# Optimization experiments

Measured on AMD Instinct MI355X. Metric: run time of the kernel, lower is better.

The kernel has to match this reference:

```python
import jax, jax.numpy as jnp
import numpy as np

K = 7            # neighborhood kernel size
HEADS = 4
DIMS = [64, 64, 64, 64]
POOL = 2
MLP_NAT = 4      # mlp_ratio for NAT layers
MLP_GA = 3       # mlp_ratio for GlobalAttention


def _ln(x, g, b, eps=1e-5):
    m = x.mean(-1, keepdims=True)
    v = ((x - m) ** 2).mean(-1, keepdims=True)
    return (x - m) * jax.lax.rsqrt(v + eps) * g + b


def _nbr(L, k):
    # NATTEN-style clamped window: start in [0, L-k]
    i = jnp.arange(L)
    start = jnp.clip(i - k // 2, 0, L - k)
    idx = start[:, None] + jnp.arange(k)          # [L,k] neighbor coords
    rel = idx - i[:, None] + (k - 1)              # [L,k] rpb index in [0,2k-2]
    return idx, rel


def _nat_attn(x, qkv_w, qkv_b, rpb, proj_w, proj_b):
    B, H, W, C = x.shape
    d = C // HEADS
    qkv = (x @ qkv_w + qkv_b).reshape(B, H, W, 3, HEADS, d)
    q = qkv[..., 0, :, :].transpose(0, 3, 1, 2, 4) * (d ** -0.5)  # [B,h,H,W,d]
    kk = qkv[..., 1, :, :].transpose(0, 3, 1, 2, 4)
    vv = qkv[..., 2, :, :].transpose(0, 3, 1, 2, 4)
    iy, ry = _nbr(H, K)
    ix, rx = _nbr(W, K)
    k_nb = kk[:, :, iy][:, :, :, :, ix]   # [B,h,H,K,W,K,d]
    v_nb = vv[:, :, iy][:, :, :, :, ix]
    attn = jnp.einsum('bhijd,bhiajcd->bhijac', q, k_nb)  # [B,h,H,W,K,K]
    bias = rpb[:, ry][:, :, :, rx]                        # [h,H,K,W,K]
    attn = attn + bias.transpose(0, 1, 3, 2, 4)[None]
    B_, h_, H_, W_ = attn.shape[:4]
    attn = jax.nn.softmax(attn.reshape(B_, h_, H_, W_, K * K), axis=-1)
    attn = attn.reshape(B_, h_, H_, W_, K, K)
    out = jnp.einsum('bhijac,bhiajcd->bhijd', attn, v_nb)
    out = out.transpose(0, 2, 3, 1, 4).reshape(B, H, W, C)
    return out @ proj_w + proj_b


def _nat_block(x, ln1g, ln1b, qw, qb, rpb, pw, pb, ln2g, ln2b, f1w, f1b, f2w, f2b):
    x = x + _nat_attn(_ln(x, ln1g, ln1b), qw, qb, rpb, pw, pb)
    h = _ln(x, ln2g, ln2b)
    h = jax.nn.gelu(h @ f1w + f1b, approximate=False) @ f2w + f2b
    return x + h


def _global_block(x, ln1g, ln1b, qw, qb, ln2g, ln2b, f1w, f1b, f2w, f2b):
    B, H, W, C = x.shape
    d = C // HEADS
    xn = _ln(x, ln1g, ln1b)
    Hp, Wp = H // POOL, W // POOL
    xa = xn.reshape(B, Hp, POOL, Wp, POOL, C).mean((2, 4)).reshape(B, Hp * Wp, C)
    N = Hp * Wp
    qkv = (xa @ qw + qb).reshape(B, N, 3, HEADS, d).transpose(2, 0, 3, 1, 4)
    q, k, v = qkv[0] * (d ** -0.5), qkv[1], qkv[2]
    attn = jax.nn.softmax(jnp.einsum('bhnd,bhmd->bhnm', q, k), axis=-1)
    o = jnp.einsum('bhnm,bhmd->bhnd', attn, v)            # [B,h,N,d]
    o = o.transpose(0, 1, 3, 2).reshape(B, C, Hp, Wp)      # (attn@v).transpose(2,3).reshape(B,C,N)
    o = jnp.repeat(jnp.repeat(o, POOL, axis=2), POOL, axis=3)  # nearest upsample
    x = x + o.transpose(0, 2, 3, 1)
    h = _ln(x, ln2g, ln2b)
    h = jax.nn.gelu(h @ f1w + f1b, approximate=False) @ f2w + f2b
    return x + h


def setup_inputs() -> dict:
    key = jax.random.key(0)
    ks = iter(jax.random.split(key, 32))
    B, H, W = 4, 56, 56
    C = DIMS[0]
    n = len(DIMS) - 1  # 3 NAT branches
    s = 0.02
    inp = {
        'x': jax.random.normal(next(ks), (B, H, W, sum(DIMS)), jnp.float32),
        'nat_ln1_g': jnp.ones((n, C)), 'nat_ln1_b': jnp.zeros((n, C)),
        'nat_qkv_w': jax.random.normal(next(ks), (n, C, 3 * C)) * s,
        'nat_qkv_b': jnp.zeros((n, 3 * C)),
        'nat_rpb': jax.random.normal(next(ks), (n, HEADS, 2 * K - 1, 2 * K - 1)) * s,
        'nat_proj_w': jax.random.normal(next(ks), (n, C, C)) * s,
        'nat_proj_b': jnp.zeros((n, C)),
        'nat_ln2_g': jnp.ones((n, C)), 'nat_ln2_b': jnp.zeros((n, C)),
        'nat_fc1_w': jax.random.normal(next(ks), (n, C, MLP_NAT * C)) * s,
        'nat_fc1_b': jnp.zeros((n, MLP_NAT * C)),
        'nat_fc2_w': jax.random.normal(next(ks), (n, MLP_NAT * C, C)) * s,
        'nat_fc2_b': jnp.zeros((n, C)),
        'ga_ln1_g': jnp.ones((C,)), 'ga_ln1_b': jnp.zeros((C,)),
        'ga_qkv_w': jax.random.normal(next(ks), (C, 3 * C)) * s,
        'ga_qkv_b': jnp.zeros((3 * C,)),
        'ga_ln2_g': jnp.ones((C,)), 'ga_ln2_b': jnp.zeros((C,)),
        'ga_fc1_w': jax.random.normal(next(ks), (C, MLP_GA * C)) * s,
        'ga_fc1_b': jnp.zeros((MLP_GA * C,)),
        'ga_fc2_w': jax.random.normal(next(ks), (MLP_GA * C, C)) * s,
        'ga_fc2_b': jnp.zeros((C,)),
    }
    return inp


def reference(x, nat_ln1_g, nat_ln1_b, nat_qkv_w, nat_qkv_b, nat_rpb, nat_proj_w,
              nat_proj_b, nat_ln2_g, nat_ln2_b, nat_fc1_w, nat_fc1_b, nat_fc2_w,
              nat_fc2_b, ga_ln1_g, ga_ln1_b, ga_qkv_w, ga_qkv_b, ga_ln2_g,
              ga_ln2_b, ga_fc1_w, ga_fc1_b, ga_fc2_w, ga_fc2_b):
    parts = jnp.split(x, np.cumsum(DIMS)[:-1].tolist(), axis=-1)
    outs = []
    for i in range(len(DIMS) - 1):
        outs.append(_nat_block(parts[i], nat_ln1_g[i], nat_ln1_b[i], nat_qkv_w[i],
                               nat_qkv_b[i], nat_rpb[i], nat_proj_w[i], nat_proj_b[i],
                               nat_ln2_g[i], nat_ln2_b[i], nat_fc1_w[i], nat_fc1_b[i],
                               nat_fc2_w[i], nat_fc2_b[i]))
    outs.append(_global_block(parts[-1], ga_ln1_g, ga_ln1_b, ga_qkv_w, ga_qkv_b,
                              ga_ln2_g, ga_ln2_b, ga_fc1_w, ga_fc1_b, ga_fc2_w, ga_fc2_b))
    return jnp.concatenate(outs, axis=-1)
```

## Files before the change

kernel.cpp:

```cpp
#include <hip/hip_runtime.h>
#include <hip/hip_bf16.h>
#include <cstdint>

namespace {

constexpr int NPIX = 12544;

typedef __attribute__((ext_vector_type(8))) short bf16x8;
typedef __attribute__((ext_vector_type(4))) float f32x4;
typedef __attribute__((ext_vector_type(16))) float f32x16;
typedef _Float16 h2 __attribute__((ext_vector_type(2)));

__device__ __forceinline__ float wsum(float v) {
#pragma unroll
  for (int m = 32; m; m >>= 1) v += __shfl_xor(v, m, 64);
  return v;
}

__device__ __forceinline__ uint16_t f2bf(float f) {
  uint32_t u = __builtin_bit_cast(uint32_t, f);
  u += 0x7fffu + ((u >> 16) & 1u);
  return (uint16_t)(u >> 16);
}
__device__ __forceinline__ uint32_t packbf(float a, float b) {
  return (uint32_t)f2bf(a) | ((uint32_t)f2bf(b) << 16);
}
__device__ __forceinline__ ushort f2h(float f) {
  _Float16 h = (_Float16)f;
  return __builtin_bit_cast(ushort, h);
}
__device__ __forceinline__ h2 bch2(uint32_t u) { return __builtin_bit_cast(h2, u); }

__device__ __forceinline__ float gelu_fast(float v) {
  float u = 0.7978845608028654f * (v + 0.044715f * v * v * v);
  float e = __expf(2.f * u);
  float th = 1.f - 2.f * __builtin_amdgcn_rcpf(e + 1.f);
  return 0.5f * v * (1.f + th);
}

__global__ __launch_bounds__(256) void k_prep(
    const float* __restrict__ nqkv, const float* __restrict__ nproj,
    const float* __restrict__ nf1, const float* __restrict__ nf2,
    const float* __restrict__ gqkv, const float* __restrict__ gf1,
    const float* __restrict__ gf2, ushort* __restrict__ wT) {
  int t = blockIdx.x * 256 + threadIdx.x;
  if (t >= 201728) return;
  int i = t;
  if (i < 41472) {
    int br = i / 13824, r = i % 13824, n = r / 72, k = r % 72;
    wT[t] = k < 64 ? f2bf(nqkv[(br * 64 + k) * 192 + n]) : (ushort)0;
    return;
  }
  i -= 41472;
  if (i < 13824) {
    int br = i / 4608, r = i % 4608, n = r / 72, k = r % 72;
    wT[t] = k < 64 ? f2bf(nproj[(br * 64 + k) * 64 + n]) : (ushort)0;
    return;
  }
  i -= 13824;
  if (i < 55296) {
    int br = i / 18432, r = i % 18432, n = r / 72, k = r % 72;
    wT[t] = k < 64 ? f2bf(nf1[(br * 64 + k) * 256 + n]) : (ushort)0;
    return;
  }
  i -= 55296;
  if (i < 50688) {
    int br = i / 16896, r = i % 16896, n = r / 264, k = r % 264;
    wT[t] = k < 256 ? f2bf(nf2[(br * 256 + k) * 64 + n]) : (ushort)0;
    return;
  }
  i -= 50688;
  if (i < 13824) {
    int n = i / 72, k = i % 72;
    wT[t] = k < 64 ? f2bf(gqkv[k * 192 + n]) : (ushort)0;
    return;
  }
  i -= 13824;
  if (i < 13824) {
    int n = i / 72, k = i % 72;
    wT[t] = k < 64 ? f2bf(gf1[k * 192 + n]) : (ushort)0;
    return;
  }
  i -= 13824;
  {
    int n = i / 200, k = i % 200;
    wT[t] = k < 192 ? f2bf(gf2[k * 64 + n]) : (ushort)0;
  }
}

__global__ __launch_bounds__(256) void k_qkv(
    const float* __restrict__ x, const float* __restrict__ nat_ln1_g,
    const float* __restrict__ nat_ln1_b, const ushort* __restrict__ wT,
    const float* __restrict__ nat_qkv_b, ushort* __restrict__ qn,
    ushort* __restrict__ kvn, const float* __restrict__ ga_ln1_g,
    const float* __restrict__ ga_ln1_b, const float* __restrict__ ga_qkv_b,
    ushort* __restrict__ qb, ushort* __restrict__ kb, ushort* __restrict__ vT) {
  __shared__ __align__(16) ushort sA[64 * 72];
  int bid = blockIdx.x;
  int tid = threadIdx.x, lane = tid & 63, wid = tid >> 6;
  if (bid == 637) {
    for (int i = tid; i < 4096; i += 256) {
      int bh = i >> 8, rem = i & 255;
      int n = 784 + (rem >> 4), d = rem & 15;
      qb[((size_t)bh * 800 + n) * 16 + d] = 0;
      kb[((size_t)bh * 800 + n) * 16 + d] = 0;
      vT[((size_t)bh * 16 + d) * 800 + n] = 0;
    }
    return;
  }
  int lr = lane & 15, lk = (lane >> 4) * 8;
  if (bid < 588) {
    int br = bid / 196, grp = bid % 196;
    const ushort* Wg = wT + br * 13824;
    float g = nat_ln1_g[br * 64 + lane], bb = nat_ln1_b[br * 64 + lane];
#pragma unroll
    for (int i = 0; i < 16; ++i) {
      int pl = wid * 16 + i;
      float v = x[(size_t)(grp * 64 + pl) * 256 + br * 64 + lane];
      float s1 = wsum(v), s2 = wsum(v * v);
      float m = s1 * (1.f / 64.f);
      float var = s2 * (1.f / 64.f) - m * m;
      sA[pl * 72 + lane] = f2bf((v - m) * rsqrtf(var + 1e-5f) * g + bb);
    }
    __syncthreads();
    int m0 = wid * 16;
    bf16x8 a0 = *(const bf16x8*)&sA[(m0 + lr) * 72 + lk];
    bf16x8 a1 = *(const bf16x8*)&sA[(m0 + lr) * 72 + 32 + lk];
    int r0 = m0 + (lane >> 4) * 4;
#pragma unroll
    for (int nt = 0; nt < 12; ++nt) {
      int n0 = nt * 16;
      bf16x8 b0 = *(const bf16x8*)&Wg[(n0 + lr) * 72 + lk];
      bf16x8 b1 = *(const bf16x8*)&Wg[(n0 + lr) * 72 + 32 + lk];
      f32x4 acc = {0.f, 0.f, 0.f, 0.f};
      acc = __builtin_amdgcn_mfma_f32_16x16x32_bf16(a0, b0, acc, 0, 0, 0);
      acc = __builtin_amdgcn_mfma_f32_16x16x32_bf16(a1, b1, acc, 0, 0, 0);
      int col = n0 + lr;
      float bias = nat_qkv_b[br * 192 + col];
      if (nt < 4) {
        ushort* op = qn + ((size_t)br * NPIX + grp * 64 + r0) * 64 + col;
#pragma unroll
        for (int r = 0; r < 4; ++r) op[r * 64] = f2h((acc[r] + bias) * 0.25f);
      } else {
        ushort* op = kvn + ((size_t)br * NPIX + grp * 64 + r0) * 128 + (col - 64);
#pragma unroll
        for (int r = 0; r < 4; ++r) op[r * 128] = f2h(acc[r] + bias);
      }
    }
  } else {
    int g64 = bid - 588;
    const ushort* Wg = wT + 161280;
    float gg = ga_ln1_g[lane], bb = ga_ln1_b[lane];
#pragma unroll
    for (int i = 0; i < 16; ++i) {
      int tl = wid * 16 + i;
      int token = g64 * 64 + tl;
      int b = token / 784, rem2 = token % 784, hp = rem2 / 28, wp = rem2 % 28;
      float s = 0.f;
#pragma unroll
      for (int dy = 0; dy < 2; ++dy)
#pragma unroll
        for (int dxx = 0; dxx < 2; ++dxx) {
          int pix = b * 3136 + (hp * 2 + dy) * 56 + (wp * 2 + dxx);
          float v = x[(size_t)pix * 256 + 192 + lane];
          float s1 = wsum(v), s2 = wsum(v * v);
          float m = s1 * (1.f / 64.f);
          float var = s2 * (1.f / 64.f) - m * m;
          s += (v - m) * rsqrtf(var + 1e-5f) * gg + bb;
        }
      sA[tl * 72 + lane] = f2bf(0.25f * s);
    }
    __syncthreads();
    int m0 = wid * 16;
    bf16x8 a0 = *(const bf16x8*)&sA[(m0 + lr) * 72 + lk];
    bf16x8 a1 = *(const bf16x8*)&sA[(m0 + lr) * 72 + 32 + lk];
    int r0 = m0 + (lane >> 4) * 4;
#pragma unroll
    for (int nt = 0; nt < 12; ++nt) {
      int n0 = nt * 16;
      bf16x8 b0 = *(const bf16x8*)&Wg[(n0 + lr) * 72 + lk];
      bf16x8 b1 = *(const bf16x8*)&Wg[(n0 + lr) * 72 + 32 + lk];
      f32x4 acc = {0.f, 0.f, 0.f, 0.f};
      acc = __builtin_amdgcn_mfma_f32_16x16x32_bf16(a0, b0, acc, 0, 0, 0);
      acc = __builtin_amdgcn_mfma_f32_16x16x32_bf16(a1, b1, acc, 0, 0, 0);
      int col = n0 + lr;
      float bias = ga_qkv_b[col];
      int hh = (col & 63) >> 4, d = col & 15;
#pragma unroll
      for (int r = 0; r < 4; ++r) {
        int token = g64 * 64 + r0 + r;
        int b = token / 784, nn = token % 784;
        float v = acc[r] + bias;
        if (col < 64)
          qb[((size_t)(b * 4 + hh) * 800 + nn) * 16 + d] = f2bf(v * 0.25f);
        else if (col < 128)
          kb[((size_t)(b * 4 + hh) * 800 + nn) * 16 + d] = f2bf(v);
        else
          vT[((size_t)(b * 4 + hh) * 16 + d) * 800 + nn] = f2bf(v);
      }
    }
  }
}

__global__ __launch_bounds__(256) void k_attn(
    const ushort* __restrict__ qn, const ushort* __restrict__ kvn,
    const float* __restrict__ rpb, const ushort* __restrict__ wT,
    const float* __restrict__ pb, const float* __restrict__ x,
    float* __restrict__ x1, const ushort* __restrict__ qb,
    const ushort* __restrict__ kb, const ushort* __restrict__ vT,
    float* __restrict__ x1g) {
  __shared__ __align__(16) ushort sBuf[196 * 136];
  int bid = blockIdx.x;
  int tid = threadIdx.x, lane = tid & 63, wid = tid >> 6;
  if (bid < 588) {
    ushort* sKV = sBuf;
    int br = bid / 196, rem = bid % 196;
    int b = rem / 49, t = rem % 49;
    int y0 = (t / 7) * 8, x0 = (t % 7) * 8;
    int hy = min(max(y0 - 3, 0), 42), hx = min(max(x0 - 3, 0), 42);
    const ushort* kvbase = kvn + ((size_t)br * NPIX + b * 3136) * 128;
    for (int i = tid; i < 3136; i += 256) {
      int p = i >> 4, c = i & 15;
      int py = p / 14, px = p % 14;
      int gp = (hy + py) * 56 + (hx + px);
      uint4 v = *(const uint4*)&kvbase[(size_t)gp * 128 + c * 8];
      *(uint4*)&sKV[p * 136 + c * 8] = v;
    }
    __syncthreads();
    int pl = tid & 63, h = tid >> 6;
    int ly = pl >> 3, lx = pl & 7;
    int y = y0 + ly, xg = x0 + lx;
    int sy = min(max(y - 3, 0), 49), sx = min(max(xg - 3, 0), 49);
    int by = sy - hy, bx = sx - hx;
    int gpix = b * 3136 + y * 56 + xg;
    const ushort* qp = qn + ((size_t)br * NPIX + gpix) * 64 + h * 16;
    uint4 qv0 = *(const uint4*)&qp[0];
    uint4 qv1 = *(const uint4*)&qp[8];
    h2 q[8] = {bch2(qv0.x), bch2(qv0.y), bch2(qv0.z), bch2(qv0.w),
               bch2(qv1.x), bch2(qv1.y), bch2(qv1.z), bch2(qv1.w)};
    const float* rp = rpb + (br * 4 + h) * 169 + (sy - y + 6) * 13 + (sx - xg + 6);
    float m = -1e30f, l = 0.f;
    h2 acc[8];
    h2 z = {(_Float16)0.f, (_Float16)0.f};
#pragma unroll
    for (int i = 0; i < 8; ++i) acc[i] = z;
    for (int a = 0; a < 7; ++a) {
      const ushort* krow = &sKV[((by + a) * 14 + bx) * 136 + h * 16];
      for (int c = 0; c < 7; ++c) {
        const ushort* kp = krow + c * 136;
        uint4 k0 = *(const uint4*)&kp[0];
        uint4 k1 = *(const uint4*)&kp[8];
        h2 d = z;
        d = bch2(k0.x) * q[0] + d;
        d = bch2(k0.y) * q[1] + d;
        d = bch2(k0.z) * q[2] + d;
        d = bch2(k0.w) * q[3] + d;
        d = bch2(k1.x) * q[4] + d;
        d = bch2(k1.y) * q[5] + d;
        d = bch2(k1.z) * q[6] + d;
        d = bch2(k1.w) * q[7] + d;
        float sd = (float)d[0] + (float)d[1] + rp[a * 13 + c];
        if (sd > m) {
          float sc = __expf(m - sd);
          m = sd; l *= sc;
          h2 sc2 = {(_Float16)sc, (_Float16)sc};
#pragma unroll
          for (int i = 0; i < 8; ++i) acc[i] = acc[i] * sc2;
        }
        float p = __expf(sd - m);
        l += p;
        h2 p2 = {(_Float16)p, (_Float16)p};
        uint4 v0 = *(const uint4*)&kp[64];
        uint4 v1 = *(const uint4*)&kp[72];
        acc[0] = bch2(v0.x) * p2 + acc[0];
        acc[1] = bch2(v0.y) * p2 + acc[1];
        acc[2] = bch2(v0.z) * p2 + acc[2];
        acc[3] = bch2(v0.w) * p2 + acc[3];
        acc[4] = bch2(v1.x) * p2 + acc[4];
        acc[5] = bch2(v1.y) * p2 + acc[5];
        acc[6] = bch2(v1.z) * p2 + acc[6];
        acc[7] = bch2(v1.w) * p2 + acc[7];
      }
    }
    float inv = 1.f / l;
    __syncthreads();
    ushort* sAp = sBuf;
    uint32_t* ao = (uint32_t*)&sAp[pl * 72 + h * 16];
#pragma unroll
    for (int i = 0; i < 8; ++i)
      ao[i] = packbf((float)acc[i][0] * inv, (float)acc[i][1] * inv);
    __syncthreads();
    const ushort* Wp = wT + 41472 + br * 4608;
    int lr = lane & 15, lk = (lane >> 4) * 8;
    int m0 = wid * 16;
    bf16x8 a0 = *(const bf16x8*)&sAp[(m0 + lr) * 72 + lk];
    bf16x8 a1 = *(const bf16x8*)&sAp[(m0 + lr) * 72 + 32 + lk];
    int r0 = m0 + (lane >> 4) * 4;
#pragma unroll
    for (int nt = 0; nt < 4; ++nt) {
      int n0 = nt * 16;
      bf16x8 b0 = *(const bf16x8*)&Wp[(n0 + lr) * 72 + lk];
      bf16x8 b1 = *(const bf16x8*)&Wp[(n0 + lr) * 72 + 32 + lk];
      f32x4 oacc = {0.f, 0.f, 0.f, 0.f};
      oacc = __builtin_amdgcn_mfma_f32_16x16x32_bf16(a0, b0, oacc, 0, 0, 0);
      oacc = __builtin_amdgcn_mfma_f32_16x16x32_bf16(a1, b1, oacc, 0, 0, 0);
      int col = n0 + lr;
      float bias = pb[br * 64 + col];
#pragma unroll
      for (int r = 0; r < 4; ++r) {
        int rr = r0 + r;
        int gp2 = b * 3136 + (y0 + (rr >> 3)) * 56 + (x0 + (rr & 7));
        x1[((size_t)br * NPIX + gp2) * 64 + col] =
            oacc[r] + bias + x[(size_t)gp2 * 256 + br * 64 + col];
      }
    }
  } else {
    int wt = (bid - 588) * 4 + wid;
    int bh = wt / 25, qt = wt % 25;
    int h = bh & 3, b = bh >> 2;
    int qrow = lane & 31, hi = lane >> 5;
    int dmod = lane & 15;
    const ushort* qbase = qb + (size_t)bh * 800 * 16;
    const ushort* kbase = kb + (size_t)bh * 800 * 16;
    const ushort* vbase = vT + (size_t)bh * 16 * 800 + (size_t)dmod * 800;
    bf16x8 qf = *(const bf16x8*)&qbase[(qt * 32 + qrow) * 16 + hi * 8];
    float m = -1e30f, l = 0.f;
    f32x16 acc_o;
#pragma unroll
    for (int r = 0; r < 16; ++r) acc_o[r] = 0.f;
    bf16x8 kf = *(const bf16x8*)&kbase[(0 + qrow) * 16 + hi * 8];
    bf16x8 vf0 = *(const bf16x8*)&vbase[0 + hi * 8];
    bf16x8 vf1 = *(const bf16x8*)&vbase[16 + hi * 8];
    for (int kt = 0; kt < 25; ++kt) {
      int nb = (kt < 24 ? kt + 1 : 24) * 32;
      bf16x8 nkf = *(const bf16x8*)&kbase[(nb + qrow) * 16 + hi * 8];
      bf16x8 nvf0 = *(const bf16x8*)&vbase[nb + hi * 8];
      bf16x8 nvf1 = *(const bf16x8*)&vbase[nb + 16 + hi * 8];
      f32x16 zero;
#pragma unroll
      for (int r = 0; r < 16; ++r) zero[r] = 0.f;
      f32x16 st = __builtin_amdgcn_mfma_f32_32x32x16_bf16(kf, qf, zero, 0, 0, 0);
      float s[16];
#pragma unroll
      for (int r = 0; r < 16; ++r) s[r] = st[r];
      if (kt == 24) {
#pragma unroll
        for (int r = 8; r < 16; ++r) s[r] = -1e30f;
      }
      float tm = s[0];
#pragma unroll
      for (int r = 1; r < 16; ++r) tm = fmaxf(tm, s[r]);
      tm = fmaxf(tm, __shfl_xor(tm, 32, 64));
      if (__any(tm > m + 8.f)) {
        float mn = fmaxf(m, tm);
        float sc = __expf(m - mn);
        l *= sc;
        m = mn;
#pragma unroll
        for (int r = 0; r < 16; ++r) {
          int row = (r & 3) + 4 * hi + 8 * (r >> 2);
          float scr = __shfl(sc, row, 64);
          acc_o[r] *= scr;
        }
      }
      uint32_t pk[8];
      float ps = 0.f;
#pragma unroll
      for (int i = 0; i < 8; ++i) {
        float p0 = __expf(s[2 * i] - m), p1 = __expf(s[2 * i + 1] - m);
        ps += p0 + p1;
        pk[i] = packbf(p0, p1);
      }
      l += ps;
#pragma unroll
      for (int t = 0; t < 2; ++t) {
        uint32_t c0 = pk[4 * t + 0], c1 = pk[4 * t + 1];
        uint32_t c2 = pk[4 * t + 2], c3 = pk[4 * t + 3];
        uint32_t b00 = __shfl((int)c0, qrow, 64), b02 = __shfl((int)c2, qrow, 64);
        uint32_t b10 = __shfl((int)c1, qrow, 64), b12 = __shfl((int)c3, qrow, 64);
        uint32_t b20 = __shfl((int)c0, qrow + 32, 64), b22 = __shfl((int)c2, qrow + 32, 64);
        uint32_t b30 = __shfl((int)c1, qrow + 32, 64), b32 = __shfl((int)c3, qrow + 32, 64);
        union { uint32_t u[4]; bf16x8 v; } pa;
        pa.u[0] = hi ? b02 : b00;
        pa.u[1] = hi ? b12 : b10;
        pa.u[2] = hi ? b22 : b20;
        pa.u[3] = hi ? b32 : b30;
        acc_o = __builtin_amdgcn_mfma_f32_32x32x16_bf16(pa.v, (t ? vf1 : vf0),
                                                        acc_o, 0, 0, 0);
      }
      kf = nkf; vf0 = nvf0; vf1 = nvf1;
    }
    l += __shfl_xor(l, 32, 64);
    float inv = 1.f / l;
#pragma unroll
    for (int r = 0; r < 16; ++r) {
      int row = (r & 3) + 4 * hi + 8 * (r >> 2);
      float invr = __shfl(inv, row, 64);
      int n = qt * 32 + row;
      if (n < 784 && qrow < 16) {
        float o = acc_o[r] * invr;
        int hp = n / 28, wp = n % 28;
        int ch = h * 16 + dmod;
#pragma unroll
        for (int dy = 0; dy < 2; ++dy)
#pragma unroll
          for (int dxx = 0; dxx < 2; ++dxx) {
            int pix = b * 3136 + (hp * 2 + dy) * 56 + (wp * 2 + dxx);
            x1g[(size_t)pix * 64 + ch] = x[(size_t)pix * 256 + 192 + ch] + o;
          }
      }
    }
  }
}

template <bool NAT>
__device__ __forceinline__ void mlp_body(
    int br, int grp, ushort* sX, ushort* sH,
    const float* __restrict__ x1, const ushort* __restrict__ W1,
    const ushort* __restrict__ W2, const float* __restrict__ B1,
    const float* __restrict__ B2, const float* __restrict__ G,
    const float* __restrict__ Bt, float* __restrict__ out) {
  constexpr int H1 = NAT ? 256 : 192;
  constexpr int K2P = NAT ? 264 : 200;
  constexpr int KB = H1 / 32;
  int tid = threadIdx.x, lane = tid & 63, wid = tid >> 6;
  const float* xin = x1 + ((size_t)br * NPIX + grp * 64) * 64;
  float g = G[lane], bb = Bt[lane];
#pragma unroll
  for (int i = 0; i < 16; ++i) {
    int pl = wid * 16 + i;
    float v = xin[pl * 64 + lane];
    float s1 = wsum(v), s2 = wsum(v * v);
    float m = s1 * (1.f / 64.f);
    float var = s2 * (1.f / 64.f) - m * m;
    sX[pl * 72 + lane] = f2bf((v - m) * rsqrtf(var + 1e-5f) * g + bb);
  }
  __syncthreads();
  int lr = lane & 15, lk = (lane >> 4) * 8;
  int mbase = (wid & 1) * 16;
  int r0 = (lane >> 4) * 4;
  bf16x8 a0[2], a1[2];
#pragma unroll
  for (int mh = 0; mh < 2; ++mh) {
    int m0 = mh * 32 + mbase;
    a0[mh] = *(const bf16x8*)&sX[(m0 + lr) * 72 + lk];
    a1[mh] = *(const bf16x8*)&sX[(m0 + lr) * 72 + 32 + lk];
  }
#pragma unroll
  for (int t2 = 0; t2 < H1 / 32; ++t2) {
    int n0 = ((wid >> 1) + 2 * t2) * 16;
    bf16x8 b0 = *(const bf16x8*)&W1[(n0 + lr) * 72 + lk];
    bf16x8 b1 = *(const bf16x8*)&W1[(n0 + lr) * 72 + 32 + lk];
    int col = n0 + lr;
    float b1v = B1[col];
#pragma unroll
    for (int mh = 0; mh < 2; ++mh) {
      f32x4 acc = {0.f, 0.f, 0.f, 0.f};
      acc = __builtin_amdgcn_mfma_f32_16x16x32_bf16(a0[mh], b0, acc, 0, 0, 0);
      acc = __builtin_amdgcn_mfma_f32_16x16x32_bf16(a1[mh], b1, acc, 0, 0, 0);
      int m0 = mh * 32 + mbase;
#pragma unroll
      for (int r = 0; r < 4; ++r)
        sH[(m0 + r0 + r) * K2P + col] = f2bf(gelu_fast(acc[r] + b1v));
    }
  }
  __syncthreads();
#pragma unroll
  for (int mh = 0; mh < 2; ++mh) {
    int m0 = mh * 32 + mbase;
    bf16x8 af[KB];
#pragma unroll
    for (int kb = 0; kb < KB; ++kb)
      af[kb] = *(const bf16x8*)&sH[(m0 + lr) * K2P + kb * 32 + lk];
#pragma unroll
    for (int u = 0; u < 2; ++u) {
      int n0 = ((wid >> 1) + 2 * u) * 16;
      f32x4 acc = {0.f, 0.f, 0.f, 0.f};
#pragma unroll
      for (int kb = 0; kb < KB; ++kb) {
        bf16x8 bf = *(const bf16x8*)&W2[(n0 + lr) * K2P + kb * 32 + lk];
        acc = __builtin_amdgcn_mfma_f32_16x16x32_bf16(af[kb], bf, acc, 0, 0, 0);
      }
      int col = n0 + lr;
      float b2v = B2[col];
#pragma unroll
      for (int r = 0; r < 4; ++r) {
        int p = m0 + r0 + r;
        int pix = grp * 64 + p;
        out[(size_t)pix * 256 + br * 64 + col] = xin[p * 64 + col] + acc[r] + b2v;
      }
    }
  }
}

__global__ __launch_bounds__(256) void k_mlp(
    const float* __restrict__ x1, const float* __restrict__ nat_ln2_g,
    const float* __restrict__ nat_ln2_b, const ushort* __restrict__ wT,
    const float* __restrict__ nat_f1b, const float* __restrict__ nat_f2b,
    const float* __restrict__ ga_ln2_g, const float* __restrict__ ga_ln2_b,
    const float* __restrict__ ga_f1b, const float* __restrict__ ga_f2b,
    float* __restrict__ out) {
  __shared__ __align__(16) ushort sX[64 * 72];
  __shared__ __align__(16) ushort sH[64 * 264];
  int bid = blockIdx.x;
  if (bid < 588) {
    int br = bid / 196, grp = bid % 196;
    mlp_body<true>(br, grp, sX, sH, x1, wT + 55296 + br * 18432,
                   wT + 110592 + br * 16896, nat_f1b + br * 256,
                   nat_f2b + br * 64, nat_ln2_g + br * 64, nat_ln2_b + br * 64,
                   out);
  } else {
    int grp = bid - 588;
    mlp_body<false>(3, grp, sX, sH, x1, wT + 175104, wT + 188928, ga_f1b,
                    ga_f2b, ga_ln2_g, ga_ln2_b, out);
  }
}

}

extern "C" void kernel_launch(void* const* d_in, const int* in_sizes, int n_in,
                              void* d_out, int out_size, void* d_ws, size_t ws_size,
                              hipStream_t stream) {
  const float* x = (const float*)d_in[0];
  const float* nat_ln1_g = (const float*)d_in[1];
  const float* nat_ln1_b = (const float*)d_in[2];
  const float* nat_qkv_w = (const float*)d_in[3];
  const float* nat_qkv_b = (const float*)d_in[4];
  const float* nat_rpb = (const float*)d_in[5];
  const float* nat_proj_w = (const float*)d_in[6];
  const float* nat_proj_b = (const float*)d_in[7];
  const float* nat_ln2_g = (const float*)d_in[8];
  const float* nat_ln2_b = (const float*)d_in[9];
  const float* nat_fc1_w = (const float*)d_in[10];
  const float* nat_fc1_b = (const float*)d_in[11];
  const float* nat_fc2_w = (const float*)d_in[12];
  const float* nat_fc2_b = (const float*)d_in[13];
  const float* ga_ln1_g = (const float*)d_in[14];
  const float* ga_ln1_b = (const float*)d_in[15];
  const float* ga_qkv_w = (const float*)d_in[16];
  const float* ga_qkv_b = (const float*)d_in[17];
  const float* ga_ln2_g = (const float*)d_in[18];
  const float* ga_ln2_b = (const float*)d_in[19];
  const float* ga_fc1_w = (const float*)d_in[20];
  const float* ga_fc1_b = (const float*)d_in[21];
  const float* ga_fc2_w = (const float*)d_in[22];
  const float* ga_fc2_b = (const float*)d_in[23];

  uint8_t* w8 = (uint8_t*)d_ws;
  ushort* qn  = (ushort*)w8;
  ushort* kvn = (ushort*)(w8 + 4816896);
  float*  x1  = (float*)(w8 + 14450688);
  ushort* wT  = (ushort*)(w8 + 27295744);
  ushort* qgb = (ushort*)(w8 + 27699200);
  ushort* kgb = (ushort*)(w8 + 28108800);
  ushort* vgT = (ushort*)(w8 + 28518400);

  k_prep<<<dim3(789), dim3(256), 0, stream>>>(nat_qkv_w, nat_proj_w, nat_fc1_w,
                                              nat_fc2_w, ga_qkv_w, ga_fc1_w,
                                              ga_fc2_w, wT);
  k_qkv<<<dim3(638), dim3(256), 0, stream>>>(x, nat_ln1_g, nat_ln1_b, wT,
                                             nat_qkv_b, qn, kvn, ga_ln1_g,
                                             ga_ln1_b, ga_qkv_b, qgb, kgb, vgT);
  k_attn<<<dim3(688), dim3(256), 0, stream>>>(qn, kvn, nat_rpb, wT, nat_proj_b,
                                              x, x1, qgb, kgb, vgT,
                                              x1 + (size_t)3 * NPIX * 64);
  k_mlp<<<dim3(784), dim3(256), 0, stream>>>(x1, nat_ln2_g, nat_ln2_b, wT,
                                             nat_fc1_b, nat_fc2_b, ga_ln2_g,
                                             ga_ln2_b, ga_fc1_b, ga_fc2_b,
                                             (float*)d_out);
}
```

Before: 85.20 us.

## Use two-pass softmax in neighborhood attention and XOR-swizzle MLP hidden smem

Replaces the online softmax in the NAT attention loop with a two-pass scheme: all 49 scores go into a fully unrolled register array, then a max and an exp/accumulate pass over V. This removes the data-dependent rescale branch and the per-step accumulator rescaling, at the cost of 49 extra live registers per thread and possibly lower occupancy. Separately, the MLP hidden-activation shared buffer is XOR-swizzled by row group on both write and read to reduce LDS bank conflicts.

```diff
diff --git a/kernel.cpp b/kernel.cpp
--- a/kernel.cpp
+++ b/kernel.cpp
@@ -239,13 +239,14 @@
     h2 q[8] = {bch2(qv0.x), bch2(qv0.y), bch2(qv0.z), bch2(qv0.w),
                bch2(qv1.x), bch2(qv1.y), bch2(qv1.z), bch2(qv1.w)};
     const float* rp = rpb + (br * 4 + h) * 169 + (sy - y + 6) * 13 + (sx - xg + 6);
-    float m = -1e30f, l = 0.f;
-    h2 acc[8];
     h2 z = {(_Float16)0.f, (_Float16)0.f};
-#pragma unroll
-    for (int i = 0; i < 8; ++i) acc[i] = z;
+    float s[49];
+    float mx = -1e30f;
+#pragma unroll
     for (int a = 0; a < 7; ++a) {
       const ushort* krow = &sKV[((by + a) * 14 + bx) * 136 + h * 16];
+      const float* rpa = rp + a * 13;
+#pragma unroll
       for (int c = 0; c < 7; ++c) {
         const ushort* kp = krow + c * 136;
         uint4 k0 = *(const uint4*)&kp[0];
@@ -259,19 +260,26 @@
         d = bch2(k1.y) * q[5] + d;
         d = bch2(k1.z) * q[6] + d;
         d = bch2(k1.w) * q[7] + d;
-        float sd = (float)d[0] + (float)d[1] + rp[a * 13 + c];
-        if (sd > m) {
-          float sc = __expf(m - sd);
-          m = sd; l *= sc;
-          h2 sc2 = {(_Float16)sc, (_Float16)sc};
-#pragma unroll
-          for (int i = 0; i < 8; ++i) acc[i] = acc[i] * sc2;
-        }
-        float p = __expf(sd - m);
+        float sd = (float)d[0] + (float)d[1] + rpa[c];
+        s[a * 7 + c] = sd;
+        mx = fmaxf(mx, sd);
+      }
+    }
+    float l = 0.f;
+    h2 acc[8];
+#pragma unroll
+    for (int i = 0; i < 8; ++i) acc[i] = z;
+#pragma unroll
+    for (int a = 0; a < 7; ++a) {
+      const ushort* vrow = &sKV[((by + a) * 14 + bx) * 136 + h * 16 + 64];
+#pragma unroll
+      for (int c = 0; c < 7; ++c) {
+        float p = __expf(s[a * 7 + c] - mx);
         l += p;
         h2 p2 = {(_Float16)p, (_Float16)p};
-        uint4 v0 = *(const uint4*)&kp[64];
-        uint4 v1 = *(const uint4*)&kp[72];
+        const ushort* vp = vrow + c * 136;
+        uint4 v0 = *(const uint4*)&vp[0];
+        uint4 v1 = *(const uint4*)&vp[8];
         acc[0] = bch2(v0.x) * p2 + acc[0];
         acc[1] = bch2(v0.y) * p2 + acc[1];
         acc[2] = bch2(v0.z) * p2 + acc[2];
@@ -460,8 +468,11 @@
       acc = __builtin_amdgcn_mfma_f32_16x16x32_bf16(a1[mh], b1, acc, 0, 0, 0);
       int m0 = mh * 32 + mbase;
 #pragma unroll
-      for (int r = 0; r < 4; ++r)
-        sH[(m0 + r0 + r) * K2P + col] = f2bf(gelu_fast(acc[r] + b1v));
+      for (int r = 0; r < 4; ++r) {
+        int row = m0 + r0 + r;
+        sH[row * K2P + (col ^ (((row >> 2) & 3) << 3))] =
+            f2bf(gelu_fast(acc[r] + b1v));
+      }
     }
   }
   __syncthreads();
@@ -470,8 +481,11 @@
     int m0 = mh * 32 + mbase;
     bf16x8 af[KB];
 #pragma unroll
-    for (int kb = 0; kb < KB; ++kb)
-      af[kb] = *(const bf16x8*)&sH[(m0 + lr) * K2P + kb * 32 + lk];
+    for (int kb = 0; kb < KB; ++kb) {
+      int arow = m0 + lr;
+      af[kb] = *(const bf16x8*)&sH[arow * K2P +
+                                   ((kb * 32 + lk) ^ (((arow >> 2) & 3) << 3))];
+    }
 #pragma unroll
     for (int u = 0; u < 2; ++u) {
       int n0 = ((wid >> 1) + 2 * u) * 16;
```

Result: no change. 85.15 us (-0.1%).
